# Performance work log

Measured on AMD Instinct MI355X. Metric: run time of the kernel, lower is better.

## Reference

```python
import jax, jax.numpy as jnp
import numpy as np

HIDDEN = 2048
N_HEADS = 16
N_KV = 4
HEAD_DIM = 128
B, T = 2, 2048


def setup_inputs() -> dict:
    key = jax.random.key(0)
    k1, k2, k3, k4 = jax.random.split(key, 4)
    x = jax.random.normal(k1, (B, T, HIDDEN), dtype=jnp.float32)
    # linear weights stored [out, in] like torch; we apply x @ W.T
    w_q = jax.random.normal(k2, (N_HEADS * HEAD_DIM, HIDDEN), dtype=jnp.float32) * (HIDDEN ** -0.5)
    w_kv = jax.random.normal(k3, (2 * N_KV * HEAD_DIM, HIDDEN), dtype=jnp.float32) * (HIDDEN ** -0.5)
    w_o = jax.random.normal(k4, (HIDDEN, N_HEADS * HEAD_DIM), dtype=jnp.float32) * ((N_HEADS * HEAD_DIM) ** -0.5)
    return {"x": x, "w_q": w_q, "w_kv": w_kv, "w_o": w_o}


def reference(x, w_q, w_kv, w_o):
    b, t, _ = x.shape
    groups = N_HEADS // N_KV
    scale = HEAD_DIM ** -0.5

    q = (x @ w_q.T).reshape(b, t, N_HEADS, HEAD_DIM).transpose(0, 2, 1, 3)  # [B,H,T,D]
    kv = x @ w_kv.T
    k, v = jnp.split(kv, 2, axis=-1)
    k = k.reshape(b, t, N_KV, HEAD_DIM).transpose(0, 2, 1, 3)  # [B,KV,T,D]
    v = v.reshape(b, t, N_KV, HEAD_DIM).transpose(0, 2, 1, 3)
    # repeat_interleave over head dim -> [B,H,T,D]
    k = jnp.repeat(k, groups, axis=1)
    v = jnp.repeat(v, groups, axis=1)

    scores = jnp.einsum('bhqd,bhkd->bhqk', q, k) * scale  # [B,H,T,T]
    causal = jnp.triu(jnp.ones((t, t), dtype=bool), k=1)
    scores = jnp.where(causal, -jnp.inf, scores)
    weights = jax.nn.softmax(scores, axis=-1)
    out = jnp.einsum('bhqk,bhkd->bhqd', weights, v)  # [B,H,T,D]
    out = out.transpose(0, 2, 1, 3).reshape(b, t, N_HEADS * HEAD_DIM)
    return out @ w_o.T
```

## Files before the change

kernel.cpp:

```cpp
#include <hip/hip_runtime.h>

typedef short bf16x8 __attribute__((ext_vector_type(8)));
typedef float f32x4 __attribute__((ext_vector_type(4)));

__device__ __forceinline__ unsigned short f2bf(float f) {
    unsigned int u = __float_as_uint(f);
    u = (u + 0x7fff + ((u >> 16) & 1)) >> 16;
    return (unsigned short)u;
}
__device__ __forceinline__ float bf2f(short s) {
    return __uint_as_float(((unsigned int)(unsigned short)s) << 16);
}

__device__ __forceinline__ void async16(const void* g, void* l) {
    __builtin_amdgcn_global_load_lds(
        (const __attribute__((address_space(1))) void*)g,
        (__attribute__((address_space(3))) void*)l,
        16 , 0 , 0 );
}

__global__ void castk(const float* __restrict__ in, unsigned short* __restrict__ out, int n4) {
    int i = blockIdx.x * blockDim.x + threadIdx.x;
    if (i < n4) {
        float4 f = ((const float4*)in)[i];
        ushort4 u;
        u.x = f2bf(f.x); u.y = f2bf(f.y); u.z = f2bf(f.z); u.w = f2bf(f.w);
        ((ushort4*)out)[i] = u;
    }
}

template <int NREP, typename OutT>
__global__ __launch_bounds__(512, 2) void gemm8p(const unsigned short* __restrict__ A,
                                                 const unsigned short* __restrict__ B,
                                                 OutT* __restrict__ C,
                                                 int N, int K, int NT,
                                                 int ncut, float qscale) {
    constexpr int NCH = 4 + NREP;
    __shared__ __attribute__((aligned(16))) unsigned short LA[2][256 * 64];
    __shared__ __attribute__((aligned(16))) unsigned short LB[2][NREP * 64 * 64];

    const int tid  = threadIdx.x;
    const int lane = tid & 63;
    const int w    = tid >> 6;
    const int quad = lane >> 4;
    const int l16  = lane & 15;
    const int wm   = w >> 2;
    const int wn   = w & 3;
    const int m0   = blockIdx.x * 256;
    const int n0   = blockIdx.y * (NREP * 64);
    const int swz  = (l16 & 7) << 3;

    const int lr = lane >> 3;
    const int ls = lane & 7;
    const int ss = ls ^ lr;
    const unsigned short* aSrc = A + (size_t)(m0 + w * 8 + lr) * K + ss * 8;
    const unsigned short* bSrc = B + (size_t)(n0 + w * 8 + lr) * K + ss * 8;

    f32x4 acc[8][NREP] = {};

    auto stage1 = [&](int nb, int t, int si) {
        if (si >= NCH) return;
        if (si < NREP) {
            async16(bSrc + (size_t)si * 64 * K + t * 64, &LB[nb][(si * 64 + w * 8) * 64]);
        } else {
            int j = si - NREP;
            int c = (j == 0) ? 0 : (j == 1) ? 2 : (j == 2) ? 1 : 3;
            async16(aSrc + (size_t)c * 64 * K + t * 64, &LA[nb][(c * 64 + w * 8) * 64]);
        }
    };

    auto readA = [&](int cur, int q, bf16x8 af[2][2]) {
#pragma unroll
        for (int mi = 0; mi < 2; ++mi)
#pragma unroll
            for (int kk = 0; kk < 2; ++kk)
                af[mi][kk] = *(const bf16x8*)&LA[cur][(size_t)(wm * 128 + (q * 2 + mi) * 16 + l16) * 64
                                                      + ((kk * 32 + quad * 8) ^ swz)];
    };

    auto domfma = [&](int q, bf16x8 af[2][2], bf16x8 (&bf)[NREP][2]) {
        __builtin_amdgcn_s_setprio(1);
#pragma unroll
        for (int mi = 0; mi < 2; ++mi)
#pragma unroll
            for (int n = 0; n < NREP; ++n)
#pragma unroll
                for (int kk = 0; kk < 2; ++kk)
                    acc[q * 2 + mi][n] = __builtin_amdgcn_mfma_f32_16x16x32_bf16(
                        af[mi][kk], bf[n][kk], acc[q * 2 + mi][n], 0, 0, 0);
        __builtin_amdgcn_s_setprio(0);
    };

    auto ktile = [&](int cur, int tn, bool last) {
        bf16x8 bf[NREP][2];
        bf16x8 af0[2][2], af1[2][2], af2[2][2], af3[2][2];
        asm volatile("s_waitcnt vmcnt(2)" ::: "memory");
        if (!last) { stage1(cur ^ 1, tn, 0); stage1(cur ^ 1, tn, 1); }
        asm volatile("s_barrier" ::: "memory");
#pragma unroll
        for (int n = 0; n < NREP; ++n)
#pragma unroll
            for (int kk = 0; kk < 2; ++kk)
                bf[n][kk] = *(const bf16x8*)&LB[cur][(size_t)(wn * (NREP * 16) + n * 16 + l16) * 64
                                                     + ((kk * 32 + quad * 8) ^ swz)];
        readA(cur, 0, af0);
        domfma(0, af0, bf);
        readA(cur, 1, af1);
        if (!last) { stage1(cur ^ 1, tn, 2); stage1(cur ^ 1, tn, 3); }
        asm volatile("s_barrier" ::: "memory");
        domfma(1, af1, bf);
        if (last) asm volatile("s_waitcnt vmcnt(0)" ::: "memory");
        else      asm volatile("s_waitcnt vmcnt(4)" ::: "memory");
        if (!last) { stage1(cur ^ 1, tn, 4); stage1(cur ^ 1, tn, 5); }
        asm volatile("s_barrier" ::: "memory");
        readA(cur, 2, af2);
        domfma(2, af2, bf);
        readA(cur, 3, af3);
        if (!last) { stage1(cur ^ 1, tn, 6); stage1(cur ^ 1, tn, 7); }
        asm volatile("s_barrier" ::: "memory");
        domfma(3, af3, bf);
    };

#pragma unroll
    for (int s = 0; s < NCH; ++s) stage1(0, 0, s);

    int cur = 0;
    for (int t = 0; t < NT - 1; ++t) {
        ktile(cur, t + 1, false);
        cur ^= 1;
    }
    ktile(cur, 0, true);

#pragma unroll
    for (int m = 0; m < 8; ++m) {
        int row = m0 + wm * 128 + m * 16 + quad * 4;
#pragma unroll
        for (int n = 0; n < NREP; ++n) {
            int col = n0 + wn * (NREP * 16) + n * 16 + l16;
            f32x4 v = acc[m][n];
            float s = (col < ncut) ? qscale : 1.0f;
#pragma unroll
            for (int j = 0; j < 4; ++j) {
                float vj = v[j] * s;
                if constexpr (sizeof(OutT) == 4)
                    C[(size_t)(row + j) * N + col] = vj;
                else
                    C[(size_t)(row + j) * N + col] = f2bf(vj);
            }
        }
    }
}

__global__ __launch_bounds__(256) void transpose_v(const unsigned short* __restrict__ QKV,
                                                   unsigned short* __restrict__ Vt) {
    __shared__ unsigned short Ls[64 * 136];
    const int tid = threadIdx.x;
    const int k0  = blockIdx.x * 64;
    const int b   = blockIdx.y >> 2;
    const int kvh = blockIdx.y & 3;

#pragma unroll
    for (int pass = 0; pass < 4; ++pass) {
        int c = tid + pass * 256;
        int key = c >> 4, dc = (c & 15) * 8;
        bf16x8 v = *(const bf16x8*)(QKV + (size_t)(b * 2048 + k0 + key) * 3072 + 2560 + kvh * 128 + dc);
        *(bf16x8*)&Ls[key * 136 + dc] = v;
    }
    __syncthreads();
#pragma unroll
    for (int pass = 0; pass < 4; ++pass) {
        int c = tid + pass * 256;
        int d = c >> 3, kc = (c & 7) * 8;
        bf16x8 v;
#pragma unroll
        for (int i = 0; i < 8; ++i) v[i] = (short)Ls[(kc + i) * 136 + d];
        *(bf16x8*)(Vt + ((size_t)(b * 4 + kvh) * 128 + d) * 2048 + k0 + kc) = v;
    }
}

__global__ __launch_bounds__(256, 2) void attn_fwd5(const unsigned short* __restrict__ QKV,
                                                    const unsigned short* __restrict__ Vt,
                                                    unsigned short* __restrict__ Opart,
                                                    float* __restrict__ lpart) {
    __shared__ __attribute__((aligned(16))) unsigned short Ks[2][64 * 128];
    __shared__ __attribute__((aligned(16))) unsigned short Vs[2][128 * 64];
    __shared__ __attribute__((aligned(16))) unsigned short Ps[4][32 * 64];

    const int tid  = threadIdx.x;
    const int lane = tid & 63;
    const int w    = tid >> 6;
    const int quad = lane >> 4;
    const int l16  = lane & 15;
    const int swz  = (l16 & 7) << 3;

    const int hb   = blockIdx.x;
    const int h    = hb & 15;
    const int b    = hb >> 4;
    const int y    = blockIdx.y;
    const int p    = 15 - (y >> 1);
    const int half = y & 1;
    const int kvh  = h >> 2;
    const float M_FIX = 12.0f;

    const int ntot   = p + 1;
    const int tstart = half ? ntot : 0;
    const int tend   = half ? 2 * ntot : ntot;

    const int qbase = p * 128;
    const int qw0   = qbase + w * 32;
    const int qw1   = qw0 + 16;

    bf16x8 qf[2][4];
#pragma unroll
    for (int g = 0; g < 2; ++g)
#pragma unroll
        for (int kd = 0; kd < 4; ++kd)
            qf[g][kd] = *(const bf16x8*)(QKV + (size_t)(b * 2048 + qw0 + g * 16 + l16) * 3072
                                         + h * 128 + kd * 32 + quad * 8);

    f32x4 oacc[2][8] = {};
    float rs[2][4] = {};

    const unsigned short* gk[4];
    const unsigned short* gv[4];
#pragma unroll
    for (int pp = 0; pp < 4; ++pp) {
        int r  = (4 * w + pp) * 4 + (lane >> 4);
        int s  = lane & 15;
        int sp = (s & 8) | ((s ^ r) & 7);
        gk[pp] = QKV + (size_t)(b * 2048 + r) * 3072 + 2048 + kvh * 128 + sp * 8;
        int d  = (4 * w + pp) * 8 + (lane >> 3);
        int sv = (lane & 7) ^ (d & 7);
        gv[pp] = Vt + ((size_t)(b * 4 + kvh) * 128 + d) * 2048 + sv * 8;
    }

    unsigned short* Pw = &Ps[w][0];

    auto stage = [&](int nb, int t) {
        const size_t ko = (size_t)t * 64;
#pragma unroll
        for (int pp = 0; pp < 4; ++pp) {
            async16(gk[pp] + ko * 3072, &Ks[nb][(4 * w + pp) * 512]);
            async16(gv[pp] + ko,        &Vs[nb][(4 * w + pp) * 512]);
        }
    };

    stage(0, tstart);
    int cur = 0;

    for (int t = tstart; t < tend; ++t) {
        __syncthreads();
        if (t + 1 < tend) stage(cur ^ 1, t + 1);
        const int k0 = t * 64;

        if (k0 <= qw0 + 15) {
            const bool live1 = (k0 <= qw1 + 15);

            f32x4 sacc[2][4] = {};
            __builtin_amdgcn_s_setprio(1);
#pragma unroll
            for (int kt = 0; kt < 4; ++kt) {
                bf16x8 kf[4];
#pragma unroll
                for (int kd = 0; kd < 4; ++kd)
                    kf[kd] = *(const bf16x8*)&Ks[cur][(kt * 16 + l16) * 128
                                                      + ((kd * 32 + quad * 8) ^ swz)];
#pragma unroll
                for (int kd = 0; kd < 4; ++kd)
                    sacc[0][kt] = __builtin_amdgcn_mfma_f32_16x16x32_bf16(qf[0][kd], kf[kd], sacc[0][kt], 0, 0, 0);
                if (live1) {
#pragma unroll
                    for (int kd = 0; kd < 4; ++kd)
                        sacc[1][kt] = __builtin_amdgcn_mfma_f32_16x16x32_bf16(qf[1][kd], kf[kd], sacc[1][kt], 0, 0, 0);
                }
            }
            __builtin_amdgcn_s_setprio(0);

#pragma unroll
            for (int g = 0; g < 2; ++g) {
                if (g == 1 && !live1) continue;
                const int qwg = qw0 + g * 16;
                const bool diag = (k0 + 63 > qwg);
#pragma unroll
                for (int j = 0; j < 4; ++j) {
                    int qrow = qwg + quad * 4 + j;
                    int prow = g * 16 + quad * 4 + j;
                    int psw  = (prow & 7) << 3;
#pragma unroll
                    for (int kt = 0; kt < 4; ++kt) {
                        float pv = __expf(sacc[g][kt][j] - M_FIX);
                        if (diag) {
                            int key = k0 + kt * 16 + l16;
                            if (key > qrow) pv = 0.f;
                        }
                        rs[g][j] += pv;
                        Pw[prow * 64 + ((kt * 16 + l16) ^ psw)] = f2bf(pv);
                    }
                }
            }

            bf16x8 pf[2][2];
#pragma unroll
            for (int g = 0; g < 2; ++g) {
                if (g == 1 && !live1) continue;
#pragma unroll
                for (int ks = 0; ks < 2; ++ks)
                    pf[g][ks] = *(const bf16x8*)&Pw[(g * 16 + l16) * 64
                                                    + ((ks * 32 + quad * 8) ^ swz)];
            }
            __builtin_amdgcn_s_setprio(1);
#pragma unroll
            for (int dt = 0; dt < 8; ++dt) {
                bf16x8 vf[2];
#pragma unroll
                for (int ks = 0; ks < 2; ++ks)
                    vf[ks] = *(const bf16x8*)&Vs[cur][(dt * 16 + l16) * 64
                                                      + ((ks * 32 + quad * 8) ^ swz)];
#pragma unroll
                for (int ks = 0; ks < 2; ++ks)
                    oacc[0][dt] = __builtin_amdgcn_mfma_f32_16x16x32_bf16(pf[0][ks], vf[ks], oacc[0][dt], 0, 0, 0);
                if (live1) {
#pragma unroll
                    for (int ks = 0; ks < 2; ++ks)
                        oacc[1][dt] = __builtin_amdgcn_mfma_f32_16x16x32_bf16(pf[1][ks], vf[ks], oacc[1][dt], 0, 0, 0);
                }
            }
            __builtin_amdgcn_s_setprio(0);
        }
        cur ^= 1;
    }

#pragma unroll
    for (int g = 0; g < 2; ++g) {
#pragma unroll
        for (int j = 0; j < 4; ++j) {
            float r = rs[g][j];
#pragma unroll
            for (int off = 1; off < 16; off <<= 1)
                r += __shfl_xor(r, off, 64);
            if (l16 == 0)
                lpart[((size_t)(half * 2 + b) * 16 + h) * 2048 + qw0 + g * 16 + quad * 4 + j] = r;
        }
#pragma unroll
        for (int dt = 0; dt < 8; ++dt)
#pragma unroll
            for (int j = 0; j < 4; ++j) {
                int qrow = qw0 + g * 16 + quad * 4 + j;
                Opart[(size_t)(half * 4096 + b * 2048 + qrow) * 2048 + h * 128 + dt * 16 + l16] =
                    f2bf(oacc[g][dt][j]);
            }
    }
}

__global__ __launch_bounds__(256) void combine(const unsigned short* __restrict__ Opart,
                                               const float* __restrict__ lpart,
                                               unsigned short* __restrict__ O) {
    const int r   = blockIdx.x;
    const int b   = r >> 11, row = r & 2047;
    const int col = threadIdx.x * 8;
    const int h   = col >> 7;
    bf16x8 a = *(const bf16x8*)(Opart + (size_t)r * 2048 + col);
    bf16x8 c = *(const bf16x8*)(Opart + (size_t)(4096 + r) * 2048 + col);
    float la = lpart[((size_t)(0 * 2 + b) * 16 + h) * 2048 + row];
    float lb = lpart[((size_t)(1 * 2 + b) * 16 + h) * 2048 + row];
    float inv = 1.0f / (la + lb);
    bf16x8 o;
#pragma unroll
    for (int i = 0; i < 8; ++i)
        o[i] = (short)f2bf((bf2f(a[i]) + bf2f(c[i])) * inv);
    *(bf16x8*)(O + (size_t)r * 2048 + col) = o;
}

extern "C" void kernel_launch(void* const* d_in, const int* in_sizes, int n_in,
                              void* d_out, int out_size, void* d_ws, size_t ws_size,
                              hipStream_t stream) {
    const float* x   = (const float*)d_in[0];
    const float* wq  = (const float*)d_in[1];
    const float* wkv = (const float*)d_in[2];
    const float* wo  = (const float*)d_in[3];
    float* out = (float*)d_out;

    char* ws = (char*)d_ws;
    size_t off = 0;
    auto alloc = [&](size_t bytes) { size_t o = off; off += (bytes + 255) & ~(size_t)255; return o; };
    unsigned short* xb    = (unsigned short*)(ws + alloc((size_t)4096 * 2048 * 2));
    unsigned short* wqkvb = (unsigned short*)(ws + alloc((size_t)3072 * 2048 * 2));
    unsigned short* wob   = (unsigned short*)(ws + alloc((size_t)2048 * 2048 * 2));
    unsigned short* QKVb  = (unsigned short*)(ws + alloc((size_t)4096 * 3072 * 2));
    unsigned short* Ab    = (unsigned short*)(ws + alloc((size_t)4096 * 2048 * 2));
    unsigned short* Vtb   = (unsigned short*)(ws + alloc((size_t)2 * 4 * 128 * 2048 * 2));
    unsigned short* Opart = (unsigned short*)(ws + alloc((size_t)2 * 4096 * 2048 * 2));
    float*          lpart = (float*)(ws + alloc((size_t)2 * 2 * 16 * 2048 * 4));

    const float qscale = 0.08838834764831845f;

    castk<<<8192, 256, 0, stream>>>(x,   xb,    4096 * 2048 / 4);
    castk<<<4096, 256, 0, stream>>>(wq,  wqkvb, 2048 * 2048 / 4);
    castk<<<2048, 256, 0, stream>>>(wkv, wqkvb + (size_t)2048 * 2048, 1024 * 2048 / 4);
    castk<<<4096, 256, 0, stream>>>(wo,  wob,   2048 * 2048 / 4);

    gemm8p<4, unsigned short><<<dim3(16, 12), 512, 0, stream>>>(xb, wqkvb, QKVb, 3072, 2048, 32, 2048, qscale);

    transpose_v<<<dim3(32, 8), 256, 0, stream>>>(QKVb, Vtb);

    attn_fwd5<<<dim3(32, 32), 256, 0, stream>>>(QKVb, Vtb, Opart, lpart);
    combine<<<4096, 256, 0, stream>>>(Opart, lpart, Ab);

    gemm8p<2, float><<<dim3(16, 16), 512, 0, stream>>>(Ab, wob, out, 2048, 2048, 32, 0, 1.0f);
}
```

Baseline: 305.4 us.

## Restructure GEMM k-tile into uniform barrier-bracketed phases and retile QKV projection

The hand-pipelined GEMM k-tile loop becomes four uniform phases. Each phase reads LDS fragments, issues the next tile's async global-to-LDS loads, waits on vmcnt and lgkmcnt, and runs its MFMA block under raised priority between two barriers, with a sched_barrier to stop the compiler moving code across the boundary. The aim is a more predictable interleaving of loads and MFMAs across waves, at the cost of extra barriers per k-tile. The QKV projection also switches from NREP=4 on a 16x12 grid to NREP=3 on a 16x16 grid, giving more workgroups to fill the CUs with smaller per-block N tiles.

```diff
diff --git a/kernel.cpp b/kernel.cpp
--- a/kernel.cpp
+++ b/kernel.cpp
@@ -69,16 +69,31 @@
         }
     };
 
-    auto readA = [&](int cur, int q, bf16x8 af[2][2]) {
+    auto phase = [&](int cur, int q, bf16x8 (&bf)[NREP][2], int tn, bool last) {
+        bf16x8 af[2][2];
+        if (q == 0) {
+#pragma unroll
+            for (int n = 0; n < NREP; ++n)
+#pragma unroll
+                for (int kk = 0; kk < 2; ++kk)
+                    bf[n][kk] = *(const bf16x8*)&LB[cur][(size_t)(wn * (NREP * 16) + n * 16 + l16) * 64
+                                                         + ((kk * 32 + quad * 8) ^ swz)];
+        }
 #pragma unroll
         for (int mi = 0; mi < 2; ++mi)
 #pragma unroll
             for (int kk = 0; kk < 2; ++kk)
                 af[mi][kk] = *(const bf16x8*)&LA[cur][(size_t)(wm * 128 + (q * 2 + mi) * 16 + l16) * 64
                                                       + ((kk * 32 + quad * 8) ^ swz)];
-    };
-
-    auto domfma = [&](int q, bf16x8 af[2][2], bf16x8 (&bf)[NREP][2]) {
+        if (!last) { stage1(cur ^ 1, tn, 2 * q); stage1(cur ^ 1, tn, 2 * q + 1); }
+        if (q == 1) {
+            if (last) asm volatile("s_waitcnt vmcnt(0)" ::: "memory");
+            else      asm volatile("s_waitcnt vmcnt(4)" ::: "memory");
+        }
+        if (q == 3 && !last) asm volatile("s_waitcnt vmcnt(2)" ::: "memory");
+        __builtin_amdgcn_s_barrier();
+        asm volatile("s_waitcnt lgkmcnt(0)" ::: "memory");
+        __builtin_amdgcn_sched_barrier(0);
         __builtin_amdgcn_s_setprio(1);
 #pragma unroll
         for (int mi = 0; mi < 2; ++mi)
@@ -89,40 +104,21 @@
                     acc[q * 2 + mi][n] = __builtin_amdgcn_mfma_f32_16x16x32_bf16(
                         af[mi][kk], bf[n][kk], acc[q * 2 + mi][n], 0, 0, 0);
         __builtin_amdgcn_s_setprio(0);
+        __builtin_amdgcn_s_barrier();
     };
 
     auto ktile = [&](int cur, int tn, bool last) {
         bf16x8 bf[NREP][2];
-        bf16x8 af0[2][2], af1[2][2], af2[2][2], af3[2][2];
-        asm volatile("s_waitcnt vmcnt(2)" ::: "memory");
-        if (!last) { stage1(cur ^ 1, tn, 0); stage1(cur ^ 1, tn, 1); }
-        asm volatile("s_barrier" ::: "memory");
-#pragma unroll
-        for (int n = 0; n < NREP; ++n)
-#pragma unroll
-            for (int kk = 0; kk < 2; ++kk)
-                bf[n][kk] = *(const bf16x8*)&LB[cur][(size_t)(wn * (NREP * 16) + n * 16 + l16) * 64
-                                                     + ((kk * 32 + quad * 8) ^ swz)];
-        readA(cur, 0, af0);
-        domfma(0, af0, bf);
-        readA(cur, 1, af1);
-        if (!last) { stage1(cur ^ 1, tn, 2); stage1(cur ^ 1, tn, 3); }
-        asm volatile("s_barrier" ::: "memory");
-        domfma(1, af1, bf);
-        if (last) asm volatile("s_waitcnt vmcnt(0)" ::: "memory");
-        else      asm volatile("s_waitcnt vmcnt(4)" ::: "memory");
-        if (!last) { stage1(cur ^ 1, tn, 4); stage1(cur ^ 1, tn, 5); }
-        asm volatile("s_barrier" ::: "memory");
-        readA(cur, 2, af2);
-        domfma(2, af2, bf);
-        readA(cur, 3, af3);
-        if (!last) { stage1(cur ^ 1, tn, 6); stage1(cur ^ 1, tn, 7); }
-        asm volatile("s_barrier" ::: "memory");
-        domfma(3, af3, bf);
+        phase(cur, 0, bf, tn, last);
+        phase(cur, 1, bf, tn, last);
+        phase(cur, 2, bf, tn, last);
+        phase(cur, 3, bf, tn, last);
     };
 
 #pragma unroll
     for (int s = 0; s < NCH; ++s) stage1(0, 0, s);
+    asm volatile("s_waitcnt vmcnt(2)" ::: "memory");
+    __builtin_amdgcn_s_barrier();
 
     int cur = 0;
     for (int t = 0; t < NT - 1; ++t) {
@@ -399,7 +395,7 @@
     castk<<<2048, 256, 0, stream>>>(wkv, wqkvb + (size_t)2048 * 2048, 1024 * 2048 / 4);
     castk<<<4096, 256, 0, stream>>>(wo,  wob,   2048 * 2048 / 4);
 
-    gemm8p<4, unsigned short><<<dim3(16, 12), 512, 0, stream>>>(xb, wqkvb, QKVb, 3072, 2048, 32, 2048, qscale);
+    gemm8p<3, unsigned short><<<dim3(16, 16), 512, 0, stream>>>(xb, wqkvb, QKVb, 3072, 2048, 32, 2048, qscale);
 
     transpose_v<<<dim3(32, 8), 256, 0, stream>>>(QKVb, Vtb);
 
```

Result: faster. 290.8 us (-4.8%).
